# Kernel tuning notes

Measured on AMD Instinct MI355X. Metric: run time of the kernel, lower is better.

Reference implementation:

```python
import jax, jax.numpy as jnp
import numpy as np

HID = 768
NSPLITS = 12
HEAD_RATIO = 2
H = NSPLITS // HEAD_RATIO          # 6 attention heads
D = HID // NSPLITS                 # 64 head size
AH = H * D                         # 384 all_head_size
KS = 9                             # conv kernel size
PAD = (KS - 1) // 2
B, S = 4, 1024


def setup_inputs() -> dict:
    key = jax.random.key(0)
    ks = jax.random.split(key, 16)
    std = 0.02
    inp = {
        "Q": jax.random.normal(ks[0], (B, S, HID), jnp.float32),
        "K": jax.random.normal(ks[1], (B, S, HID), jnp.float32),
        "V": jax.random.normal(ks[2], (B, S, HID), jnp.float32),
        "td": jax.random.uniform(ks[3], (B, S), jnp.float32),
        "mask": jax.random.randint(ks[4], (B, S), 0, 2, jnp.int32),
        # projection weights, applied as x @ W (in, out)
        "Wq": jax.random.normal(ks[5], (HID, AH), jnp.float32) * std,
        "Wk": jax.random.normal(ks[6], (HID, AH), jnp.float32) * std,
        "Wv": jax.random.normal(ks[7], (HID, AH), jnp.float32) * std,
        # separable conv: depthwise (HID, KS), pointwise (AH, HID), bias (AH,)
        "dw_w": jax.random.normal(ks[8], (HID, KS), jnp.float32) * std,
        "pw_w": jax.random.normal(ks[9], (AH, HID), jnp.float32) * std,
        "sep_b": jnp.zeros((AH,), jnp.float32),
        # conv_kernel_layer Linear(AH -> H*KS)
        "ck_W": jax.random.normal(ks[10], (AH, H * KS), jnp.float32) * std,
        "ck_b": jnp.zeros((H * KS,), jnp.float32),
        # conv_out_layer Linear(HID -> AH)
        "co_W": jax.random.normal(ks[11], (HID, AH), jnp.float32) * std,
        "co_b": jnp.zeros((AH,), jnp.float32),
        # gammas init to zeros as in torch module
        "gammas": jnp.zeros((H, 1, 1), jnp.float32),
    }
    return inp


def dist_func(scores, td, am, gammas):
    # scores: [B,H,S,S]; am: [B,1,1,S] bool key mask; entirely non-differentiable.
    s = scores.shape[-1]
    dt = scores.dtype
    amf = am.astype(dt)
    p = jax.nn.softmax(jnp.where(am, scores, -1e8), axis=-1) * amf
    distcum = jnp.cumsum(p, axis=-1)
    disttotal = jnp.sum(p, axis=-1, keepdims=True)
    # |j - i| position distance
    pos = jnp.abs(jnp.arange(s)[None, :] - jnp.arange(s)[:, None]).astype(dt)
    dist_scores = jnp.sqrt(jnp.clip((disttotal - distcum) * pos[None, None], 0.0, None))
    gamma = -jax.nn.softplus(gammas)[None]  # (1,H,1,1)
    total_effect = jnp.clip(jnp.exp(dist_scores * gamma), 1e-5, 1e5)
    # time-distance effect on strictly-lower-triangular positions
    tdn = td / jnp.maximum(jnp.linalg.norm(td, axis=-1, keepdims=True), 1e-12)
    td_scores = jnp.broadcast_to(tdn[:, None, None, :], scores.shape)
    td_sm = jax.nn.softmax(jnp.where(am, td_scores, -1e4), axis=-1)
    lower = jnp.tril(jnp.ones((s, s), dt), -1)  # (triu == 0)
    return jax.lax.stop_gradient(total_effect - td_sm * lower[None, None])


def reference(Q, K, V, td, mask, Wq, Wk, Wv, dw_w, pw_w, sep_b, ck_W, ck_b, co_W, co_b, gammas):
    b, s, hid = Q.shape
    mq = Q @ Wq  # (B,S,AH)
    mk = K @ Wk
    mv = V @ Wv
    # SeparableConv1D over sequence dim of K
    x = jnp.transpose(K, (0, 2, 1))  # (B,HID,S)
    dw = jax.lax.conv_general_dilated(
        x, dw_w[:, None, :], window_strides=(1,), padding=[(PAD, PAD)],
        feature_group_count=hid, dimension_numbers=("NCH", "OIH", "NCH"))
    pw = jnp.einsum("bcs,oc->bos", dw, pw_w) + sep_b[None, :, None]
    mkc = jnp.transpose(pw, (0, 2, 1))  # (B,S,AH)

    q = mq.reshape(b, s, H, D).transpose(0, 2, 1, 3)
    k = mk.reshape(b, s, H, D).transpose(0, 2, 1, 3)
    v = mv.reshape(b, s, H, D).transpose(0, 2, 1, 3)

    # dynamic span convolution
    conv_attn = mkc * mq                                   # (B,S,AH)
    ck = (conv_attn @ ck_W + ck_b).reshape(b, s, H, KS)
    ck = jax.nn.softmax(ck, axis=-1)                       # per-position kernel
    co = V @ co_W + co_b                                   # (B,S,AH)
    co_pad = jnp.pad(co, ((0, 0), (PAD, PAD), (0, 0)))
    idx = jnp.arange(s)[:, None] + jnp.arange(KS)[None, :]  # (S,KS)
    unf = co_pad[:, idx, :].reshape(b, s, KS, H, D)         # sliding window gather
    conv_out = jnp.einsum("bskhd,bshk->bshd", unf, ck)      # (B,S,H,D)

    # attention with distance decay
    scores = jnp.einsum("bhid,bhjd->bhij", q, k) / np.float32(np.sqrt(D))
    am = (mask[:, None, None, :] != 0)  # (B,1,1,S) key mask
    total_effect = dist_func(scores, td, am, gammas)
    scores = jnp.where(am, scores * total_effect, -1e8)
    probs = jax.nn.softmax(scores, axis=-1)
    ctx = jnp.einsum("bhij,bhjd->bhid", probs, v).transpose(0, 2, 1, 3)  # (B,S,H,D)

    out = jnp.concatenate([ctx, conv_out], axis=2).reshape(b, s, HEAD_RATIO * AH)
    return out
```

## Files before the change

kernel.cpp:

```cpp
#include <hip/hip_runtime.h>
#include <hip/hip_bf16.h>

#define HIDC 768
#define Hh   6
#define Dd   64
#define AHc  384
#define KSc  9
#define PADc 4
#define Bb   4
#define Ss   1024
#define MRr  (Bb * Ss)

typedef __attribute__((ext_vector_type(8))) __bf16 bf16x8;
typedef __attribute__((ext_vector_type(4))) __bf16 bf16x4;
typedef __attribute__((ext_vector_type(4))) float  f32x4;

__device__ __forceinline__ void gl_lds16(const void* g, void* l) {
    __builtin_amdgcn_global_load_lds(
        (const __attribute__((address_space(1))) void*)g,
        (__attribute__((address_space(3))) void*)l, 16, 0, 0);
}

__device__ __forceinline__ void split8(const float* p, bf16x8& hi, bf16x8& lo) {
    float4 x0 = *(const float4*)p;
    float4 x1 = *(const float4*)(p + 4);
    float xs[8] = {x0.x, x0.y, x0.z, x0.w, x1.x, x1.y, x1.z, x1.w};
#pragma unroll
    for (int e = 0; e < 8; ++e) {
        __bf16 hv = (__bf16)xs[e];
        hi[e] = hv;
        lo[e] = (__bf16)(xs[e] - (float)hv);
    }
}

__device__ __forceinline__ void split8r(const float* xs, bf16x8& hi, bf16x8& lo) {
#pragma unroll
    for (int e = 0; e < 8; ++e) {
        __bf16 hv = (__bf16)xs[e];
        hi[e] = hv;
        lo[e] = (__bf16)(xs[e] - (float)hv);
    }
}

__device__ __forceinline__ bf16x8 cvt8(const float* p) {
    float4 x0 = *(const float4*)p;
    float4 x1 = *(const float4*)(p + 4);
    float xs[8] = {x0.x, x0.y, x0.z, x0.w, x1.x, x1.y, x1.z, x1.w};
    bf16x8 h;
#pragma unroll
    for (int e = 0; e < 8; ++e) h[e] = (__bf16)xs[e];
    return h;
}

__global__ __launch_bounds__(256) void k_pre(
        const float* __restrict__ Wq, const float* __restrict__ Wk,
        const float* __restrict__ Wv, const float* __restrict__ coW,
        const float* __restrict__ pww, const float* __restrict__ cob,
        const float* __restrict__ sepb, const float* __restrict__ td,
        const int* __restrict__ mask, const float* __restrict__ Kin,
        const float* __restrict__ dww, const float* __restrict__ Q,
        const float* __restrict__ V,
        __bf16* __restrict__ Whi, __bf16* __restrict__ Wlo,
        float* __restrict__ biasb, float* __restrict__ td_sm,
        __bf16* __restrict__ dwbf, __bf16* __restrict__ qbf,
        __bf16* __restrict__ vbf) {
    __shared__ float shmem[64 * 65];
    int bid = blockIdx.x;
    int tid = threadIdx.x;
    if (bid < 288) {
        int z = bid / 72, rem = bid % 72;
        int n0 = (rem % 6) * 64, k0 = (rem / 6) * 64;
        const float* src = (z == 0) ? Wq : (z == 1) ? Wk : (z == 2) ? Wv : coW;
        float (*tile)[65] = (float(*)[65])shmem;
        int r = tid >> 2, cq = tid & 3;
#pragma unroll
        for (int e = 0; e < 4; ++e) {
            float4 v = *(const float4*)&src[(size_t)(k0 + r) * AHc + n0 + cq * 16 + e * 4];
            tile[r][cq * 16 + e * 4 + 0] = v.x;
            tile[r][cq * 16 + e * 4 + 1] = v.y;
            tile[r][cq * 16 + e * 4 + 2] = v.z;
            tile[r][cq * 16 + e * 4 + 3] = v.w;
        }
        __syncthreads();
        float x[16];
#pragma unroll
        for (int e = 0; e < 16; ++e) x[e] = tile[cq * 16 + e][r];
        bf16x8 h0, l0, h1, l1;
        split8r(x, h0, l0);
        split8r(x + 8, h1, l1);
        size_t dst = ((size_t)(z * AHc + n0 + r)) * HIDC + k0 + cq * 16;
        *(bf16x8*)(Whi + dst)     = h0;
        *(bf16x8*)(Whi + dst + 8) = h1;
        *(bf16x8*)(Wlo + dst)     = l0;
        *(bf16x8*)(Wlo + dst + 8) = l1;
        return;
    }
    if (bid < 432) {
        int idx = (bid - 288) * 256 + tid;
        bf16x8 hi, lo;
        split8(pww + (size_t)idx * 8, hi, lo);
        size_t dst = (size_t)4 * AHc * HIDC + (size_t)idx * 8;
        *(bf16x8*)(Whi + dst) = hi;
        *(bf16x8*)(Wlo + dst) = lo;
        return;
    }
    if (bid < 440) {
        int idx = (bid - 432) * 256 + tid;
        if (idx < 5 * AHc) {
            int z = idx / AHc, n = idx % AHc;
            biasb[idx] = (z == 3) ? cob[n] : (z == 4) ? sepb[n] : 0.f;
        }
        return;
    }
    if (bid < 444) {
        int b = bid - 440;
        float* red = shmem;
        float* tv  = shmem + 256;
        float ls = 0.f;
        for (int j = tid; j < Ss; j += 256) {
            float v = td[b * Ss + j];
            tv[j] = v;
            ls += v * v;
        }
        red[tid] = ls; __syncthreads();
        for (int s = 128; s > 0; s >>= 1) { if (tid < s) red[tid] += red[tid + s]; __syncthreads(); }
        float norm = fmaxf(sqrtf(red[0]), 1e-12f);
        __syncthreads();
        float lm = -3e38f;
        for (int j = tid; j < Ss; j += 256) {
            float v = mask[b * Ss + j] ? tv[j] / norm : -1e4f;
            tv[j] = v;
            lm = fmaxf(lm, v);
        }
        red[tid] = lm; __syncthreads();
        for (int s = 128; s > 0; s >>= 1) { if (tid < s) red[tid] = fmaxf(red[tid], red[tid + s]); __syncthreads(); }
        float m = red[0]; __syncthreads();
        float lsum = 0.f;
        for (int j = tid; j < Ss; j += 256) {
            float e = expf(tv[j] - m);
            tv[j] = e;
            lsum += e;
        }
        red[tid] = lsum; __syncthreads();
        for (int s = 128; s > 0; s >>= 1) { if (tid < s) red[tid] += red[tid + s]; __syncthreads(); }
        float inv = 1.f / red[0];
        __syncthreads();
        for (int j = tid; j < Ss; j += 256)
            td_sm[b * Ss + j] = tv[j] * inv;
        return;
    }
    int db = bid - 444;
    if (db < 3072) {
        int idx = db * 256 + tid;
        int c4 = idx % (HIDC / 4);
        int s  = (idx / (HIDC / 4)) % Ss;
        int b  = idx / ((HIDC / 4) * Ss);
        int c  = c4 * 4;
        float wv[4][KSc];
#pragma unroll
        for (int j = 0; j < 4; ++j)
#pragma unroll
            for (int k = 0; k < KSc; ++k) wv[j][k] = dww[(c + j) * KSc + k];
        float4 acc = {0.f, 0.f, 0.f, 0.f};
#pragma unroll
        for (int k = 0; k < KSc; ++k) {
            int sp = s + k - PADc;
            if (sp >= 0 && sp < Ss) {
                float4 v = *(const float4*)&Kin[(size_t)(b * Ss + sp) * HIDC + c];
                acc.x += v.x * wv[0][k]; acc.y += v.y * wv[1][k];
                acc.z += v.z * wv[2][k]; acc.w += v.w * wv[3][k];
            }
        }
        bf16x4 o = {(__bf16)acc.x, (__bf16)acc.y, (__bf16)acc.z, (__bf16)acc.w};
        *(bf16x4*)(dwbf + (size_t)idx * 4) = o;
    } else {
        const int n8 = MRr * HIDC / 8;
        int idx = (db - 3072) * 256 + tid;
        if (idx < n8) {
            *(bf16x8*)(qbf + (size_t)idx * 8) = cvt8(Q + (size_t)idx * 8);
        } else {
            int i = idx - n8;
            *(bf16x8*)(vbf + (size_t)i * 8) = cvt8(V + (size_t)i * 8);
        }
    }
}

__global__ __launch_bounds__(256) void k_gemm5(
        const __bf16* __restrict__ qbf, const float* __restrict__ Kin,
        const __bf16* __restrict__ vbf, const __bf16* __restrict__ dwbf,
        const __bf16* __restrict__ Whi, const __bf16* __restrict__ Wlo,
        const float* __restrict__ biasb, float* __restrict__ Call,
        __bf16* __restrict__ kh, __bf16* __restrict__ kl,
        __bf16* __restrict__ qh, __bf16* __restrict__ vt) {
    __shared__ __attribute__((aligned(16))) __bf16 As [128 * 32];
    __shared__ __attribute__((aligned(16))) __bf16 BsH[128 * 32];
    __shared__ __attribute__((aligned(16))) __bf16 BsL[128 * 32];

    int wg = blockIdx.x + 3 * (blockIdx.y + 32 * blockIdx.z);
    int n2 = (wg & 7) * 60 + (wg >> 3);
    int bxx = n2 % 3, byy = (n2 / 3) % 32, z = n2 / 96;

    int m0 = byy * 128, n0 = bxx * 128;
    int tid = threadIdx.x;
    int wave = tid >> 6, lane = tid & 63, quad = lane >> 4, l15 = lane & 15;

    int lrow = lane >> 2;
    int lswz = 8 * ((lane & 3) ^ (lrow & 3));

    int brow = wave * 32 + lrow;
    const __bf16* BhG0 = Whi + ((size_t)(z * AHc + n0 + brow)) * HIDC + lswz;
    const __bf16* BhG1 = BhG0 + (size_t)16 * HIDC;
    const __bf16* BlG0 = Wlo + ((size_t)(z * AHc + n0 + brow)) * HIDC + lswz;
    const __bf16* BlG1 = BlG0 + (size_t)16 * HIDC;
    __bf16* BhL0 = BsH + (wave * 2 + 0) * 512;
    __bf16* BhL1 = BsH + (wave * 2 + 1) * 512;
    __bf16* BlL0 = BsL + (wave * 2 + 0) * 512;
    __bf16* BlL1 = BsL + (wave * 2 + 1) * 512;

    const __bf16* Abf = (z == 0) ? qbf : (z == 4) ? dwbf : vbf;
    const __bf16* AG0 = Abf + ((size_t)(m0 + wave * 32 + lrow)) * HIDC + lswz;
    const __bf16* AG1 = AG0 + (size_t)16 * HIDC;
    __bf16* AL0 = As + (wave * 2 + 0) * 512;
    __bf16* AL1 = As + (wave * 2 + 1) * 512;

    int sr = tid >> 1;
    int sk = (tid & 1) * 16;
    const float* Arow = Kin + (size_t)(m0 + sr) * HIDC + sk;
    int g0 = sk >> 3;
    int d0 = sr * 32 + ((g0       ^ (sr & 3)) * 8);
    int d1 = sr * 32 + (((g0 + 1) ^ (sr & 3)) * 8);

    int swz = (quad ^ (l15 & 3)) * 8;
    f32x4 acc[4][4] = {};

    for (int k0 = 0; k0 < HIDC; k0 += 32) {
        if (z == 1) {
            const float* ap = Arow + k0;
            *(bf16x8*)&As[d0] = cvt8(ap);
            *(bf16x8*)&As[d1] = cvt8(ap + 8);
        } else {
            gl_lds16(AG0 + k0, AL0);
            gl_lds16(AG1 + k0, AL1);
        }
        gl_lds16(BhG0 + k0, BhL0);
        gl_lds16(BhG1 + k0, BhL1);
        gl_lds16(BlG0 + k0, BlL0);
        gl_lds16(BlG1 + k0, BlL1);
        __syncthreads();

        int mrow = (wave >> 1) * 64 + l15;
        int nrow = (wave & 1) * 64 + l15;
        bf16x8 ah[4], bh[4], bl[4];
#pragma unroll
        for (int mt = 0; mt < 4; ++mt)
            ah[mt] = *(bf16x8*)&As[(mrow + mt * 16) * 32 + swz];
#pragma unroll
        for (int nt = 0; nt < 4; ++nt) {
            bh[nt] = *(bf16x8*)&BsH[(nrow + nt * 16) * 32 + swz];
            bl[nt] = *(bf16x8*)&BsL[(nrow + nt * 16) * 32 + swz];
        }
#pragma unroll
        for (int mt = 0; mt < 4; ++mt)
#pragma unroll
            for (int nt = 0; nt < 4; ++nt) {
                acc[mt][nt] = __builtin_amdgcn_mfma_f32_16x16x32_bf16(ah[mt], bh[nt], acc[mt][nt], 0, 0, 0);
                acc[mt][nt] = __builtin_amdgcn_mfma_f32_16x16x32_bf16(ah[mt], bl[nt], acc[mt][nt], 0, 0, 0);
            }
        __syncthreads();
    }

    if (z == 1) {
#pragma unroll
        for (int nt = 0; nt < 4; ++nt) {
            int n = n0 + (wave & 1) * 64 + nt * 16 + l15;
#pragma unroll
            for (int mt = 0; mt < 4; ++mt) {
#pragma unroll
                for (int r = 0; r < 4; ++r) {
                    int m = m0 + (wave >> 1) * 64 + mt * 16 + quad * 4 + r;
                    float v = acc[mt][nt][r];
                    __bf16 hv = (__bf16)v;
                    kh[(size_t)m * AHc + n] = hv;
                    kl[(size_t)m * AHc + n] = (__bf16)(v - (float)hv);
                }
            }
        }
    } else if (z == 2) {
        int b = m0 >> 10;
#pragma unroll
        for (int nt = 0; nt < 4; ++nt) {
            int n = (wave & 1) * 64 + nt * 16 + l15;
            int gn = n0 + n;
            int h = gn >> 6, d = gn & 63;
#pragma unroll
            for (int mt = 0; mt < 4; ++mt) {
                int m = m0 + (wave >> 1) * 64 + mt * 16 + quad * 4;
                int s = m & (Ss - 1);
                bf16x4 o = {(__bf16)acc[mt][nt][0], (__bf16)acc[mt][nt][1],
                            (__bf16)acc[mt][nt][2], (__bf16)acc[mt][nt][3]};
                *(bf16x4*)&vt[((size_t)((b * Hh + h) * Dd + d)) * Ss + s] = o;
            }
        }
    } else if (z == 0) {
#pragma unroll
        for (int nt = 0; nt < 4; ++nt) {
            int n = n0 + (wave & 1) * 64 + nt * 16 + l15;
#pragma unroll
            for (int mt = 0; mt < 4; ++mt) {
#pragma unroll
                for (int r = 0; r < 4; ++r) {
                    int m = m0 + (wave >> 1) * 64 + mt * 16 + quad * 4 + r;
                    float v = acc[mt][nt][r];
                    Call[(size_t)m * AHc + n] = v;
                    qh[(size_t)m * AHc + n] = (__bf16)v;
                }
            }
        }
    } else {
        float* Cz = Call + (size_t)z * MRr * AHc;
        const float* bz = biasb + z * AHc;
#pragma unroll
        for (int nt = 0; nt < 4; ++nt) {
            int n = n0 + (wave & 1) * 64 + nt * 16 + l15;
            float bias = bz[n];
#pragma unroll
            for (int mt = 0; mt < 4; ++mt) {
#pragma unroll
                for (int r = 0; r < 4; ++r) {
                    int m = m0 + (wave >> 1) * 64 + mt * 16 + quad * 4 + r;
                    Cz[(size_t)m * AHc + n] = acc[mt][nt][r] + bias;
                }
            }
        }
    }
}

__global__ __launch_bounds__(256) void k_ckconv(const float* __restrict__ mkc,
                                                const float* __restrict__ mq,
                                                const float* __restrict__ ckW,
                                                const float* __restrict__ ckb,
                                                const float* __restrict__ co,
                                                float* __restrict__ out) {
    int tid = threadIdx.x;
    int lr = tid >> 6, lane = tid & 63;
    int row = blockIdx.x * 4 + lr;
    __shared__ float ca[4][AHc];
    __shared__ float ckv[4][Hh * KSc];
    for (int o = lane; o < AHc; o += 64)
        ca[lr][o] = mkc[(size_t)row * AHc + o] * mq[(size_t)row * AHc + o];
    __syncthreads();
    if (lane < Hh * KSc) {
        float acc = ckb[lane];
        for (int o = 0; o < AHc; ++o)
            acc += ca[lr][o] * ckW[o * (Hh * KSc) + lane];
        ckv[lr][lane] = acc;
    }
    __syncthreads();
    if (lane < Hh) {
        float m = -3e38f;
#pragma unroll
        for (int k = 0; k < KSc; ++k) m = fmaxf(m, ckv[lr][lane * KSc + k]);
        float e[KSc];
        float s = 0.f;
#pragma unroll
        for (int k = 0; k < KSc; ++k) { e[k] = expf(ckv[lr][lane * KSc + k] - m); s += e[k]; }
        float inv = 1.f / s;
#pragma unroll
        for (int k = 0; k < KSc; ++k) ckv[lr][lane * KSc + k] = e[k] * inv;
    }
    __syncthreads();
#pragma unroll
    for (int e = 0; e < 2; ++e) {
        int it = e * 256 + tid;
        if (it >= 4 * (AHc / 4)) break;
        int r4i = it / (AHc / 4), dq = it % (AHc / 4);
        int h = dq >> 4, d4 = dq & 15;
        int row2 = blockIdx.x * 4 + r4i;
        int s = row2 & (Ss - 1), b = row2 >> 10;
        float4 acc = {0.f, 0.f, 0.f, 0.f};
#pragma unroll
        for (int k = 0; k < KSc; ++k) {
            int sp = s + k - PADc;
            if (sp >= 0 && sp < Ss) {
                float4 v = *(const float4*)&co[(size_t)(b * Ss + sp) * AHc + h * Dd + d4 * 4];
                float wv = ckv[r4i][h * KSc + k];
                acc.x += wv * v.x; acc.y += wv * v.y; acc.z += wv * v.z; acc.w += wv * v.w;
            }
        }
        *(float4*)&out[(size_t)row2 * (2 * AHc) + AHc + h * Dd + d4 * 4] = acc;
    }
}

__device__ __forceinline__ int scix(int m, int j) {
    return m * 1024 + (j ^ (((m ^ (j >> 6)) & 7) << 2));
}

__global__ __launch_bounds__(512, 4) void k_attn(const __bf16* __restrict__ qh,
                                              const __bf16* __restrict__ kh, const __bf16* __restrict__ kl,
                                              const __bf16* __restrict__ vt,
                                              const int* __restrict__ mask,
                                              const float* __restrict__ td_sm, const float* __restrict__ gammas,
                                              float* __restrict__ out) {
    __shared__ float sc[16 * 1024];
    int wg = blockIdx.x + 64 * blockIdx.y;
    int n  = (wg & 7) * 192 + (wg >> 3);
    int bx = n & 63, by = n >> 6;
    int i0 = bx * 16;
    int h = by % Hh, b = by / Hh;
    int tid = threadIdx.x;
    int w = tid >> 6, lane = tid & 63, quad = lane >> 4, l15 = lane & 15;
    int jw = w * 128;

    bf16x8 a_hi[2];
    {
        size_t qoff = (size_t)(b * Ss + i0 + l15) * AHc + h * Dd + quad * 8;
        a_hi[0] = *(const bf16x8*)(qh + qoff);
        a_hi[1] = *(const bf16x8*)(qh + qoff + 32);
    }
#pragma unroll 4
    for (int t = 0; t < 8; ++t) {
        int jt = jw + t * 16;
        size_t koff = (size_t)(b * Ss + jt + l15) * AHc + h * Dd + quad * 8;
        f32x4 acc = {0.f, 0.f, 0.f, 0.f};
#pragma unroll
        for (int kc = 0; kc < 2; ++kc) {
            bf16x8 khv = *(const bf16x8*)(kh + koff + kc * 32);
            bf16x8 klv = *(const bf16x8*)(kl + koff + kc * 32);
            acc = __builtin_amdgcn_mfma_f32_16x16x32_bf16(a_hi[kc], khv, acc, 0, 0, 0);
            acc = __builtin_amdgcn_mfma_f32_16x16x32_bf16(a_hi[kc], klv, acc, 0, 0, 0);
        }
#pragma unroll
        for (int r = 0; r < 4; ++r)
            sc[scix(quad * 4 + r, jt + l15)] = acc[r] * 0.125f;
    }
    __syncthreads();

    const int* mrow = mask + b * Ss;
    const float* tdrow = td_sm + b * Ss;
    float gamma = -log1pf(expf(gammas[h]));
    int jb = lane << 4;
    __attribute__((aligned(16))) int marr[16];
    {
        const int4* mp = (const int4*)(mrow + jb);
#pragma unroll
        for (int k = 0; k < 4; ++k) ((int4*)marr)[k] = mp[k];
    }
    __attribute__((aligned(16))) float tdv[16];
    {
        const float4* tp = (const float4*)(tdrow + jb);
#pragma unroll
        for (int k = 0; k < 4; ++k) ((float4*)tdv)[k] = tp[k];
    }

    {
        int mA = w * 2, mB = mA + 1;
        int iA = i0 + mA, iB = i0 + mB;
        __attribute__((aligned(16))) float sA[16], sB[16];
        float pA[16], pB[16];
#pragma unroll
        for (int g = 0; g < 4; ++g) {
            *(f32x4*)(sA + 4 * g) = *(const f32x4*)&sc[scix(mA, jb + 4 * g)];
            *(f32x4*)(sB + 4 * g) = *(const f32x4*)&sc[scix(mB, jb + 4 * g)];
        }
        float mxA = -1e30f, mxB = -1e30f;
#pragma unroll
        for (int jj = 0; jj < 16; ++jj) {
            mxA = fmaxf(mxA, marr[jj] ? sA[jj] : -1e30f);
            mxB = fmaxf(mxB, marr[jj] ? sB[jj] : -1e30f);
        }
#pragma unroll
        for (int d = 1; d < 64; d <<= 1) {
            mxA = fmaxf(mxA, __shfl_xor(mxA, d));
            mxB = fmaxf(mxB, __shfl_xor(mxB, d));
        }
#pragma unroll
        for (int jj = 0; jj < 16; ++jj) {
            pA[jj] = marr[jj] ? __expf(sA[jj] - mxA) : 0.f;
            pB[jj] = marr[jj] ? __expf(sB[jj] - mxB) : 0.f;
        }
#pragma unroll
        for (int jj = 1; jj < 16; ++jj) { pA[jj] += pA[jj - 1]; pB[jj] += pB[jj - 1]; }
        float tA = pA[15], tB = pB[15];
        float incA = tA, incB = tB;
#pragma unroll
        for (int dlt = 1; dlt < 64; dlt <<= 1) {
            float vA = __shfl_up(incA, dlt);
            float vB = __shfl_up(incB, dlt);
            if (lane >= dlt) { incA += vA; incB += vB; }
        }
        float offA = incA - tA, offB = incB - tB;
        float totA = __shfl(incA, 63), totB = __shfl(incB, 63);
        float invA = 1.f / fmaxf(totA, 1e-30f), invB = 1.f / fmaxf(totB, 1e-30f);
        float mx2A = -1e30f, mx2B = -1e30f;
#pragma unroll
        for (int jj = 0; jj < 16; ++jj) {
            int j = jb + jj;
            float cumA = pA[jj] + offA, cumB = pB[jj] + offB;
            float posA = fabsf((float)(j - iA));
            float posB = fabsf((float)(j - iB));
            float dsA = sqrtf(fmaxf((totA - cumA) * invA * posA, 0.f));
            float dsB = sqrtf(fmaxf((totB - cumB) * invB * posB, 0.f));
            float teA = fminf(fmaxf(__expf(dsA * gamma), 1e-5f), 1e5f);
            float teB = fminf(fmaxf(__expf(dsB * gamma), 1e-5f), 1e5f);
            float tdj = tdv[jj];
            float multA = teA - ((j < iA) ? tdj : 0.f);
            float multB = teB - ((j < iB) ? tdj : 0.f);
            float s2A = marr[jj] ? sA[jj] * multA : -1e8f;
            float s2B = marr[jj] ? sB[jj] * multB : -1e8f;
            sA[jj] = s2A; sB[jj] = s2B;
            mx2A = fmaxf(mx2A, s2A); mx2B = fmaxf(mx2B, s2B);
        }
#pragma unroll
        for (int d = 1; d < 64; d <<= 1) {
            mx2A = fmaxf(mx2A, __shfl_xor(mx2A, d));
            mx2B = fmaxf(mx2B, __shfl_xor(mx2B, d));
        }
        float smA = 0.f, smB = 0.f;
#pragma unroll
        for (int jj = 0; jj < 16; ++jj) {
            sA[jj] = __expf(sA[jj] - mx2A); smA += sA[jj];
            sB[jj] = __expf(sB[jj] - mx2B); smB += sB[jj];
        }
#pragma unroll
        for (int d = 1; d < 64; d <<= 1) {
            smA += __shfl_xor(smA, d);
            smB += __shfl_xor(smB, d);
        }
        float i2A = 1.f / smA, i2B = 1.f / smB;
#pragma unroll
        for (int jj = 0; jj < 16; ++jj) { sA[jj] *= i2A; sB[jj] *= i2B; }
#pragma unroll
        for (int g = 0; g < 4; ++g) {
            *(f32x4*)&sc[scix(mA, jb + 4 * g)] = *(const f32x4*)(sA + 4 * g);
            *(f32x4*)&sc[scix(mB, jb + 4 * g)] = *(const f32x4*)(sB + 4 * g);
        }
    }
    __syncthreads();

    f32x4 oacc[4] = {};
    const __bf16* vtb = vt + (size_t)(b * Hh + h) * Dd * Ss;
#pragma unroll
    for (int kc = 0; kc < 4; ++kc) {
        int j0 = jw + kc * 32 + quad * 8;
        __attribute__((aligned(16))) float x[8];
        *(f32x4*)x       = *(const f32x4*)&sc[scix(l15, j0)];
        *(f32x4*)(x + 4) = *(const f32x4*)&sc[scix(l15, j0 + 4)];
        bf16x8 p_hi, p_lo;
        split8r(x, p_hi, p_lo);
#pragma unroll
        for (int nt = 0; nt < 4; ++nt) {
            int d = nt * 16 + l15;
            bf16x8 vv = *(const bf16x8*)(vtb + (size_t)d * Ss + j0);
            oacc[nt] = __builtin_amdgcn_mfma_f32_16x16x32_bf16(p_hi, vv, oacc[nt], 0, 0, 0);
            oacc[nt] = __builtin_amdgcn_mfma_f32_16x16x32_bf16(p_lo, vv, oacc[nt], 0, 0, 0);
        }
    }
    __syncthreads();
#pragma unroll
    for (int nt = 0; nt < 4; ++nt)
#pragma unroll
        for (int r = 0; r < 4; ++r)
            sc[w * 1024 + (quad * 4 + r) * 64 + nt * 16 + l15] = oacc[nt][r];
    __syncthreads();
#pragma unroll
    for (int e = 0; e < 2; ++e) {
        int idx = e * 512 + tid;
        int m = idx >> 6, dd = idx & 63;
        float v = 0.f;
#pragma unroll
        for (int ww = 0; ww < 8; ++ww) v += sc[ww * 1024 + idx];
        out[(size_t)(b * Ss + i0 + m) * (2 * AHc) + h * Dd + dd] = v;
    }
}

extern "C" void kernel_launch(void* const* d_in, const int* in_sizes, int n_in,
                              void* d_out, int out_size, void* d_ws, size_t ws_size,
                              hipStream_t stream) {
    const float* Q    = (const float*)d_in[0];
    const float* Kin  = (const float*)d_in[1];
    const float* V    = (const float*)d_in[2];
    const float* td   = (const float*)d_in[3];
    const int*   mask = (const int*)d_in[4];
    const float* Wq   = (const float*)d_in[5];
    const float* Wk   = (const float*)d_in[6];
    const float* Wv   = (const float*)d_in[7];
    const float* dww  = (const float*)d_in[8];
    const float* pww  = (const float*)d_in[9];
    const float* sepb = (const float*)d_in[10];
    const float* ckW  = (const float*)d_in[11];
    const float* ckb  = (const float*)d_in[12];
    const float* coW  = (const float*)d_in[13];
    const float* cob  = (const float*)d_in[14];
    const float* gam  = (const float*)d_in[15];
    float* out = (float*)d_out;
    float* ws = (float*)d_ws;

    float* mq    = ws;
    float* mks   = mq    + (size_t)MRr * AHc;
    float* mvs   = mks   + (size_t)MRr * AHc;
    float* co    = mvs   + (size_t)MRr * AHc;
    float* mkc   = co    + (size_t)MRr * AHc;
    float* dwr   = mkc   + (size_t)MRr * AHc;
    float* tdsm  = dwr   + (size_t)MRr * HIDC;
    float* biasb = tdsm  + (size_t)Bb * Ss;

    __bf16* dwbf = (__bf16*)dwr;
    __bf16* qbf  = (__bf16*)(dwr + (size_t)MRr * HIDC / 2);
    __bf16* kh = (__bf16*)mks;
    __bf16* kl = kh + (size_t)MRr * AHc;
    __bf16* vt = (__bf16*)mvs;
    __bf16* qh = vt + (size_t)MRr * AHc;

    __bf16* Whi = (__bf16*)d_out;
    __bf16* Wlo = Whi + (size_t)5 * AHc * HIDC;
    __bf16* vbf = Wlo + (size_t)5 * AHc * HIDC;

    k_pre<<<6588, 256, 0, stream>>>(Wq, Wk, Wv, coW, pww, cob, sepb, td, mask,
                                    Kin, dww, Q, V, Whi, Wlo, biasb, tdsm,
                                    dwbf, qbf, vbf);

    dim3 gg(AHc / 128, MRr / 128, 5);
    k_gemm5<<<gg, 256, 0, stream>>>(qbf, Kin, vbf, dwbf, Whi, Wlo, biasb, mq, kh, kl, qh, vt);

    k_ckconv<<<MRr / 4, 256, 0, stream>>>(mkc, mq, ckW, ckb, co, out);

    dim3 ga(Ss / 16, Bb * Hh);
    k_attn<<<ga, 512, 0, stream>>>(qh, kh, kl, vt, mask, tdsm, gam, out);
}
```

Measured before the change: 272.6 us.

## Keep attention scores in registers and shrink LDS to small bounce buffers

The attention kernel now keeps the 16x1024 score tile in MFMA accumulator registers instead of a 64KB shared array. Softmax, cumulative-sum and distance-decay reductions are done with 16-lane shuffles plus small per-wave shared stats arrays and extra barriers. P is converted to the PV operand layout through a small swizzled per-wave bounce buffer, and the final cross-wave reduction is staged in two halves. The aim is to cut LDS footprint (raising occupancy) and LDS traffic, at the cost of more registers, more syncs and redundant per-element divides. The ck linear loop in the conv kernel is also unrolled.

```diff
diff --git a/kernel.cpp b/kernel.cpp
--- a/kernel.cpp
+++ b/kernel.cpp
@@ -351,8 +351,10 @@
     __syncthreads();
     if (lane < Hh * KSc) {
         float acc = ckb[lane];
+        const float* wp = ckW + lane;
+#pragma unroll 8
         for (int o = 0; o < AHc; ++o)
-            acc += ca[lr][o] * ckW[o * (Hh * KSc) + lane];
+            acc += ca[lr][o] * wp[o * (Hh * KSc)];
         ckv[lr][lane] = acc;
     }
     __syncthreads();
@@ -391,17 +393,14 @@
     }
 }
 
-__device__ __forceinline__ int scix(int m, int j) {
-    return m * 1024 + (j ^ (((m ^ (j >> 6)) & 7) << 2));
-}
-
 __global__ __launch_bounds__(512, 4) void k_attn(const __bf16* __restrict__ qh,
-                                              const __bf16* __restrict__ kh, const __bf16* __restrict__ kl,
-                                              const __bf16* __restrict__ vt,
-                                              const int* __restrict__ mask,
-                                              const float* __restrict__ td_sm, const float* __restrict__ gammas,
-                                              float* __restrict__ out) {
-    __shared__ float sc[16 * 1024];
+            const __bf16* __restrict__ kh, const __bf16* __restrict__ kl,
+            const __bf16* __restrict__ vt,
+            const int* __restrict__ mask,
+            const float* __restrict__ td_sm, const float* __restrict__ gammas,
+            float* __restrict__ out) {
+    __shared__ __attribute__((aligned(16))) float bounce[8][512];
+    __shared__ float statsM[128], statsS[128], stats2[128], statsZ[128];
     int wg = blockIdx.x + 64 * blockIdx.y;
     int n  = (wg & 7) * 192 + (wg >> 3);
     int bx = n & 63, by = n >> 6;
@@ -411,142 +410,202 @@
     int w = tid >> 6, lane = tid & 63, quad = lane >> 4, l15 = lane & 15;
     int jw = w * 128;
 
-    bf16x8 a_hi[2];
+    bf16x8 a_hi0, a_hi1;
     {
         size_t qoff = (size_t)(b * Ss + i0 + l15) * AHc + h * Dd + quad * 8;
-        a_hi[0] = *(const bf16x8*)(qh + qoff);
-        a_hi[1] = *(const bf16x8*)(qh + qoff + 32);
-    }
-#pragma unroll 4
+        a_hi0 = *(const bf16x8*)(qh + qoff);
+        a_hi1 = *(const bf16x8*)(qh + qoff + 32);
+    }
+    f32x4 sreg[8];
+#pragma unroll
     for (int t = 0; t < 8; ++t) {
-        int jt = jw + t * 16;
-        size_t koff = (size_t)(b * Ss + jt + l15) * AHc + h * Dd + quad * 8;
+        size_t koff = (size_t)(b * Ss + jw + t * 16 + l15) * AHc + h * Dd + quad * 8;
+        bf16x8 kh0 = *(const bf16x8*)(kh + koff);
+        bf16x8 kl0 = *(const bf16x8*)(kl + koff);
+        bf16x8 kh1 = *(const bf16x8*)(kh + koff + 32);
+        bf16x8 kl1 = *(const bf16x8*)(kl + koff + 32);
         f32x4 acc = {0.f, 0.f, 0.f, 0.f};
-#pragma unroll
-        for (int kc = 0; kc < 2; ++kc) {
-            bf16x8 khv = *(const bf16x8*)(kh + koff + kc * 32);
-            bf16x8 klv = *(const bf16x8*)(kl + koff + kc * 32);
-            acc = __builtin_amdgcn_mfma_f32_16x16x32_bf16(a_hi[kc], khv, acc, 0, 0, 0);
-            acc = __builtin_amdgcn_mfma_f32_16x16x32_bf16(a_hi[kc], klv, acc, 0, 0, 0);
-        }
+        acc = __builtin_amdgcn_mfma_f32_16x16x32_bf16(a_hi0, kh0, acc, 0, 0, 0);
+        acc = __builtin_amdgcn_mfma_f32_16x16x32_bf16(a_hi0, kl0, acc, 0, 0, 0);
+        acc = __builtin_amdgcn_mfma_f32_16x16x32_bf16(a_hi1, kh1, acc, 0, 0, 0);
+        acc = __builtin_amdgcn_mfma_f32_16x16x32_bf16(a_hi1, kl1, acc, 0, 0, 0);
+        sreg[t] = acc;
+    }
+
+    float gamma = -log1pf(expf(gammas[h]));
+    int mbits = 0;
+    float tdv[8];
+    {
+        const int* mp = mask + b * Ss + jw + l15;
+        const float* tp = td_sm + b * Ss + jw + l15;
+#pragma unroll
+        for (int t = 0; t < 8; ++t) {
+            mbits |= (mp[t * 16] != 0) << t;
+            tdv[t] = tp[t * 16];
+        }
+    }
+#pragma unroll
+    for (int t = 0; t < 8; ++t) {
+        bool bit = (mbits >> t) & 1;
 #pragma unroll
         for (int r = 0; r < 4; ++r)
-            sc[scix(quad * 4 + r, jt + l15)] = acc[r] * 0.125f;
-    }
-    __syncthreads();
-
-    const int* mrow = mask + b * Ss;
-    const float* tdrow = td_sm + b * Ss;
-    float gamma = -log1pf(expf(gammas[h]));
-    int jb = lane << 4;
-    __attribute__((aligned(16))) int marr[16];
+            sreg[t][r] = bit ? sreg[t][r] * 0.125f : -1e30f;
+    }
     {
-        const int4* mp = (const int4*)(mrow + jb);
-#pragma unroll
-        for (int k = 0; k < 4; ++k) ((int4*)marr)[k] = mp[k];
-    }
-    __attribute__((aligned(16))) float tdv[16];
+        float pm[4];
+#pragma unroll
+        for (int r = 0; r < 4; ++r) {
+            float m0 = sreg[0][r];
+#pragma unroll
+            for (int t = 1; t < 8; ++t) m0 = fmaxf(m0, sreg[t][r]);
+#pragma unroll
+            for (int d = 1; d < 16; d <<= 1) m0 = fmaxf(m0, __shfl_xor(m0, d));
+            pm[r] = m0;
+        }
+        if (l15 == 0) {
+#pragma unroll
+            for (int r = 0; r < 4; ++r) statsM[(quad * 4 + r) * 8 + w] = pm[r];
+        }
+    }
+    __syncthreads();
+    float gmx[4];
+#pragma unroll
+    for (int r = 0; r < 4; ++r) {
+        const float* sm = &statsM[(quad * 4 + r) * 8];
+        float m0 = sm[0];
+#pragma unroll
+        for (int w2 = 1; w2 < 8; ++w2) m0 = fmaxf(m0, sm[w2]);
+        gmx[r] = m0;
+    }
+    float p[8][4];
     {
-        const float4* tp = (const float4*)(tdrow + jb);
-#pragma unroll
-        for (int k = 0; k < 4; ++k) ((float4*)tdv)[k] = tp[k];
-    }
-
-    {
-        int mA = w * 2, mB = mA + 1;
-        int iA = i0 + mA, iB = i0 + mB;
-        __attribute__((aligned(16))) float sA[16], sB[16];
-        float pA[16], pB[16];
-#pragma unroll
-        for (int g = 0; g < 4; ++g) {
-            *(f32x4*)(sA + 4 * g) = *(const f32x4*)&sc[scix(mA, jb + 4 * g)];
-            *(f32x4*)(sB + 4 * g) = *(const f32x4*)&sc[scix(mB, jb + 4 * g)];
-        }
-        float mxA = -1e30f, mxB = -1e30f;
-#pragma unroll
-        for (int jj = 0; jj < 16; ++jj) {
-            mxA = fmaxf(mxA, marr[jj] ? sA[jj] : -1e30f);
-            mxB = fmaxf(mxB, marr[jj] ? sB[jj] : -1e30f);
-        }
-#pragma unroll
-        for (int d = 1; d < 64; d <<= 1) {
-            mxA = fmaxf(mxA, __shfl_xor(mxA, d));
-            mxB = fmaxf(mxB, __shfl_xor(mxB, d));
-        }
-#pragma unroll
-        for (int jj = 0; jj < 16; ++jj) {
-            pA[jj] = marr[jj] ? __expf(sA[jj] - mxA) : 0.f;
-            pB[jj] = marr[jj] ? __expf(sB[jj] - mxB) : 0.f;
-        }
-#pragma unroll
-        for (int jj = 1; jj < 16; ++jj) { pA[jj] += pA[jj - 1]; pB[jj] += pB[jj - 1]; }
-        float tA = pA[15], tB = pB[15];
-        float incA = tA, incB = tB;
-#pragma unroll
-        for (int dlt = 1; dlt < 64; dlt <<= 1) {
-            float vA = __shfl_up(incA, dlt);
-            float vB = __shfl_up(incB, dlt);
-            if (lane >= dlt) { incA += vA; incB += vB; }
-        }
-        float offA = incA - tA, offB = incB - tB;
-        float totA = __shfl(incA, 63), totB = __shfl(incB, 63);
-        float invA = 1.f / fmaxf(totA, 1e-30f), invB = 1.f / fmaxf(totB, 1e-30f);
-        float mx2A = -1e30f, mx2B = -1e30f;
-#pragma unroll
-        for (int jj = 0; jj < 16; ++jj) {
-            int j = jb + jj;
-            float cumA = pA[jj] + offA, cumB = pB[jj] + offB;
-            float posA = fabsf((float)(j - iA));
-            float posB = fabsf((float)(j - iB));
-            float dsA = sqrtf(fmaxf((totA - cumA) * invA * posA, 0.f));
-            float dsB = sqrtf(fmaxf((totB - cumB) * invB * posB, 0.f));
-            float teA = fminf(fmaxf(__expf(dsA * gamma), 1e-5f), 1e5f);
-            float teB = fminf(fmaxf(__expf(dsB * gamma), 1e-5f), 1e5f);
-            float tdj = tdv[jj];
-            float multA = teA - ((j < iA) ? tdj : 0.f);
-            float multB = teB - ((j < iB) ? tdj : 0.f);
-            float s2A = marr[jj] ? sA[jj] * multA : -1e8f;
-            float s2B = marr[jj] ? sB[jj] * multB : -1e8f;
-            sA[jj] = s2A; sB[jj] = s2B;
-            mx2A = fmaxf(mx2A, s2A); mx2B = fmaxf(mx2B, s2B);
-        }
-#pragma unroll
-        for (int d = 1; d < 64; d <<= 1) {
-            mx2A = fmaxf(mx2A, __shfl_xor(mx2A, d));
-            mx2B = fmaxf(mx2B, __shfl_xor(mx2B, d));
-        }
-        float smA = 0.f, smB = 0.f;
-#pragma unroll
-        for (int jj = 0; jj < 16; ++jj) {
-            sA[jj] = __expf(sA[jj] - mx2A); smA += sA[jj];
-            sB[jj] = __expf(sB[jj] - mx2B); smB += sB[jj];
-        }
-#pragma unroll
-        for (int d = 1; d < 64; d <<= 1) {
-            smA += __shfl_xor(smA, d);
-            smB += __shfl_xor(smB, d);
-        }
-        float i2A = 1.f / smA, i2B = 1.f / smB;
-#pragma unroll
-        for (int jj = 0; jj < 16; ++jj) { sA[jj] *= i2A; sB[jj] *= i2B; }
-#pragma unroll
-        for (int g = 0; g < 4; ++g) {
-            *(f32x4*)&sc[scix(mA, jb + 4 * g)] = *(const f32x4*)(sA + 4 * g);
-            *(f32x4*)&sc[scix(mB, jb + 4 * g)] = *(const f32x4*)(sB + 4 * g);
-        }
-    }
-    __syncthreads();
+        float wrow[4];
+#pragma unroll
+        for (int r = 0; r < 4; ++r) {
+            float run = 0.f;
+#pragma unroll
+            for (int t = 0; t < 8; ++t) {
+                float v = __expf(sreg[t][r] - gmx[r]);
+#pragma unroll
+                for (int d = 1; d < 16; d <<= 1) {
+                    float u = __shfl_up(v, d, 16);
+                    if (l15 >= d) v += u;
+                }
+                float ct = __shfl(v, 15, 16);
+                p[t][r] = v + run;
+                run += ct;
+            }
+            wrow[r] = run;
+        }
+        if (l15 == 0) {
+#pragma unroll
+            for (int r = 0; r < 4; ++r) statsS[(quad * 4 + r) * 8 + w] = wrow[r];
+        }
+    }
+    __syncthreads();
+    float woff[4], tot[4];
+#pragma unroll
+    for (int r = 0; r < 4; ++r) {
+        const float* ss = &statsS[(quad * 4 + r) * 8];
+        float o = 0.f, t_ = 0.f;
+#pragma unroll
+        for (int w2 = 0; w2 < 8; ++w2) {
+            float v = ss[w2];
+            if (w2 < w) o += v;
+            t_ += v;
+        }
+        woff[r] = o; tot[r] = t_;
+    }
+    float mx2[4] = {-1e30f, -1e30f, -1e30f, -1e30f};
+#pragma unroll
+    for (int t = 0; t < 8; ++t) {
+        int j = jw + t * 16 + l15;
+        int bit = (mbits >> t) & 1;
+#pragma unroll
+        for (int r = 0; r < 4; ++r) {
+            int i = i0 + quad * 4 + r;
+            float inv = 1.f / fmaxf(tot[r], 1e-30f);
+            float cum = p[t][r] + woff[r];
+            float pos = fabsf((float)(j - i));
+            float ds = sqrtf(fmaxf((tot[r] - cum) * inv * pos, 0.f));
+            float te = fminf(fmaxf(__expf(ds * gamma), 1e-5f), 1e5f);
+            float mult = te - ((j < i) ? tdv[t] : 0.f);
+            float s2 = bit ? sreg[t][r] * mult : -1e8f;
+            sreg[t][r] = s2;
+            mx2[r] = fmaxf(mx2[r], s2);
+        }
+    }
+#pragma unroll
+    for (int r = 0; r < 4; ++r) {
+#pragma unroll
+        for (int d = 1; d < 16; d <<= 1) mx2[r] = fmaxf(mx2[r], __shfl_xor(mx2[r], d));
+    }
+    if (l15 == 0) {
+#pragma unroll
+        for (int r = 0; r < 4; ++r) stats2[(quad * 4 + r) * 8 + w] = mx2[r];
+    }
+    __syncthreads();
+    float gm2[4];
+#pragma unroll
+    for (int r = 0; r < 4; ++r) {
+        const float* s2p = &stats2[(quad * 4 + r) * 8];
+        float m0 = s2p[0];
+#pragma unroll
+        for (int w2 = 1; w2 < 8; ++w2) m0 = fmaxf(m0, s2p[w2]);
+        gm2[r] = m0;
+    }
+    float smr[4] = {0.f, 0.f, 0.f, 0.f};
+#pragma unroll
+    for (int t = 0; t < 8; ++t)
+#pragma unroll
+        for (int r = 0; r < 4; ++r) {
+            float e = __expf(sreg[t][r] - gm2[r]);
+            sreg[t][r] = e;
+            smr[r] += e;
+        }
+#pragma unroll
+    for (int r = 0; r < 4; ++r) {
+#pragma unroll
+        for (int d = 1; d < 16; d <<= 1) smr[r] += __shfl_xor(smr[r], d);
+    }
+    if (l15 == 0) {
+#pragma unroll
+        for (int r = 0; r < 4; ++r) statsZ[(quad * 4 + r) * 8 + w] = smr[r];
+    }
+    __syncthreads();
+#pragma unroll
+    for (int r = 0; r < 4; ++r) {
+        const float* zp = &statsZ[(quad * 4 + r) * 8];
+        float z = 0.f;
+#pragma unroll
+        for (int w2 = 0; w2 < 8; ++w2) z += zp[w2];
+        float inv2 = 1.f / z;
+#pragma unroll
+        for (int t = 0; t < 8; ++t) sreg[t][r] *= inv2;
+    }
 
     f32x4 oacc[4] = {};
     const __bf16* vtb = vt + (size_t)(b * Hh + h) * Dd * Ss;
+    float* myb = &bounce[w][0];
 #pragma unroll
     for (int kc = 0; kc < 4; ++kc) {
-        int j0 = jw + kc * 32 + quad * 8;
+#pragma unroll
+        for (int half = 0; half < 2; ++half) {
+            int jl = half * 16 + l15;
+#pragma unroll
+            for (int r = 0; r < 4; ++r) {
+                int m = quad * 4 + r;
+                int gi = (jl >> 2) ^ (m & 7);
+                myb[m * 32 + gi * 4 + (jl & 3)] = sreg[kc * 2 + half][r];
+            }
+        }
+        __syncthreads();
         __attribute__((aligned(16))) float x[8];
-        *(f32x4*)x       = *(const f32x4*)&sc[scix(l15, j0)];
-        *(f32x4*)(x + 4) = *(const f32x4*)&sc[scix(l15, j0 + 4)];
+        *(f32x4*)x       = *(const f32x4*)&myb[l15 * 32 + (((quad * 2)     ^ (l15 & 7)) * 4)];
+        *(f32x4*)(x + 4) = *(const f32x4*)&myb[l15 * 32 + (((quad * 2 + 1) ^ (l15 & 7)) * 4)];
         bf16x8 p_hi, p_lo;
         split8r(x, p_hi, p_lo);
+        int j0 = jw + kc * 32 + quad * 8;
 #pragma unroll
         for (int nt = 0; nt < 4; ++nt) {
             int d = nt * 16 + l15;
@@ -554,21 +613,32 @@
             oacc[nt] = __builtin_amdgcn_mfma_f32_16x16x32_bf16(p_hi, vv, oacc[nt], 0, 0, 0);
             oacc[nt] = __builtin_amdgcn_mfma_f32_16x16x32_bf16(p_lo, vv, oacc[nt], 0, 0, 0);
         }
-    }
-    __syncthreads();
-#pragma unroll
-    for (int nt = 0; nt < 4; ++nt)
-#pragma unroll
-        for (int r = 0; r < 4; ++r)
-            sc[w * 1024 + (quad * 4 + r) * 64 + nt * 16 + l15] = oacc[nt][r];
+        __syncthreads();
+    }
+
+    float* seg = (float*)bounce;
+    if (w < 4) {
+#pragma unroll
+        for (int nt = 0; nt < 4; ++nt)
+#pragma unroll
+            for (int r = 0; r < 4; ++r)
+                seg[w * 1024 + (quad * 4 + r) * 64 + nt * 16 + l15] = oacc[nt][r];
+    }
+    __syncthreads();
+    if (w >= 4) {
+        int s4 = w - 4;
+#pragma unroll
+        for (int nt = 0; nt < 4; ++nt)
+#pragma unroll
+            for (int r = 0; r < 4; ++r)
+                seg[s4 * 1024 + (quad * 4 + r) * 64 + nt * 16 + l15] += oacc[nt][r];
+    }
     __syncthreads();
 #pragma unroll
     for (int e = 0; e < 2; ++e) {
         int idx = e * 512 + tid;
         int m = idx >> 6, dd = idx & 63;
-        float v = 0.f;
-#pragma unroll
-        for (int ww = 0; ww < 8; ++ww) v += sc[ww * 1024 + idx];
+        float v = seg[idx] + seg[1024 + idx] + seg[2048 + idx] + seg[3072 + idx];
         out[(size_t)(b * Ss + i0 + m) * (2 * AHc) + h * Dd + dd] = v;
     }
 }
```

Result: slower. 285.7 us (+4.8%).

## Merge dynamic-span conv into attention launch and pack key mask into bitmask

Applied to the files above, without the earlier changes.

The separate k_ckconv launch is removed. Its work now runs as extra blocks (blockIdx.y >= 24) of the attention kernel, with 8 rows per block and the shared score buffer reused for scratch. This saves a kernel launch and lets the conv blocks overlap with the attention blocks. In the attention path the 16-entry int mask array is packed into a bit mask, and masked scores are pre-set once, which cuts register use and per-element selects. The risk is that the conv blocks inherit the attention kernel's 512-thread shape and large LDS allocation, which could lower occupancy for that work.

```diff
diff --git a/kernel.cpp b/kernel.cpp
--- a/kernel.cpp
+++ b/kernel.cpp
@@ -335,79 +335,83 @@
     }
 }
 
-__global__ __launch_bounds__(256) void k_ckconv(const float* __restrict__ mkc,
-                                                const float* __restrict__ mq,
-                                                const float* __restrict__ ckW,
-                                                const float* __restrict__ ckb,
-                                                const float* __restrict__ co,
-                                                float* __restrict__ out) {
-    int tid = threadIdx.x;
-    int lr = tid >> 6, lane = tid & 63;
-    int row = blockIdx.x * 4 + lr;
-    __shared__ float ca[4][AHc];
-    __shared__ float ckv[4][Hh * KSc];
-    for (int o = lane; o < AHc; o += 64)
-        ca[lr][o] = mkc[(size_t)row * AHc + o] * mq[(size_t)row * AHc + o];
-    __syncthreads();
-    if (lane < Hh * KSc) {
-        float acc = ckb[lane];
-        for (int o = 0; o < AHc; ++o)
-            acc += ca[lr][o] * ckW[o * (Hh * KSc) + lane];
-        ckv[lr][lane] = acc;
-    }
-    __syncthreads();
-    if (lane < Hh) {
-        float m = -3e38f;
-#pragma unroll
-        for (int k = 0; k < KSc; ++k) m = fmaxf(m, ckv[lr][lane * KSc + k]);
-        float e[KSc];
-        float s = 0.f;
-#pragma unroll
-        for (int k = 0; k < KSc; ++k) { e[k] = expf(ckv[lr][lane * KSc + k] - m); s += e[k]; }
-        float inv = 1.f / s;
-#pragma unroll
-        for (int k = 0; k < KSc; ++k) ckv[lr][lane * KSc + k] = e[k] * inv;
-    }
-    __syncthreads();
-#pragma unroll
-    for (int e = 0; e < 2; ++e) {
-        int it = e * 256 + tid;
-        if (it >= 4 * (AHc / 4)) break;
-        int r4i = it / (AHc / 4), dq = it % (AHc / 4);
-        int h = dq >> 4, d4 = dq & 15;
-        int row2 = blockIdx.x * 4 + r4i;
-        int s = row2 & (Ss - 1), b = row2 >> 10;
-        float4 acc = {0.f, 0.f, 0.f, 0.f};
-#pragma unroll
-        for (int k = 0; k < KSc; ++k) {
-            int sp = s + k - PADc;
-            if (sp >= 0 && sp < Ss) {
-                float4 v = *(const float4*)&co[(size_t)(b * Ss + sp) * AHc + h * Dd + d4 * 4];
-                float wv = ckv[r4i][h * KSc + k];
-                acc.x += wv * v.x; acc.y += wv * v.y; acc.z += wv * v.z; acc.w += wv * v.w;
-            }
-        }
-        *(float4*)&out[(size_t)row2 * (2 * AHc) + AHc + h * Dd + d4 * 4] = acc;
-    }
-}
-
 __device__ __forceinline__ int scix(int m, int j) {
     return m * 1024 + (j ^ (((m ^ (j >> 6)) & 7) << 2));
 }
 
-__global__ __launch_bounds__(512, 4) void k_attn(const __bf16* __restrict__ qh,
-                                              const __bf16* __restrict__ kh, const __bf16* __restrict__ kl,
-                                              const __bf16* __restrict__ vt,
-                                              const int* __restrict__ mask,
-                                              const float* __restrict__ td_sm, const float* __restrict__ gammas,
-                                              float* __restrict__ out) {
+__global__ __attribute__((amdgpu_flat_work_group_size(512, 512), amdgpu_waves_per_eu(4, 4)))
+void k_attnck(const __bf16* __restrict__ qh,
+              const __bf16* __restrict__ kh, const __bf16* __restrict__ kl,
+              const __bf16* __restrict__ vt,
+              const int* __restrict__ mask,
+              const float* __restrict__ td_sm, const float* __restrict__ gammas,
+              const float* __restrict__ mkc, const float* __restrict__ mq,
+              const float* __restrict__ ckW, const float* __restrict__ ckb,
+              const float* __restrict__ co,
+              float* __restrict__ out) {
     __shared__ float sc[16 * 1024];
+    int tid = threadIdx.x;
+
+    if (blockIdx.y >= 24) {
+        int cb = blockIdx.x + 64 * (blockIdx.y - 24);
+        int lr = tid >> 6, lane = tid & 63;
+        int row = cb * 8 + lr;
+        float* ca  = sc;
+        float* ckv = sc + 8 * AHc;
+        for (int o = lane; o < AHc; o += 64)
+            ca[lr * AHc + o] = mkc[(size_t)row * AHc + o] * mq[(size_t)row * AHc + o];
+        __syncthreads();
+        if (lane < Hh * KSc) {
+            float acc = ckb[lane];
+            const float* wp = ckW + lane;
+#pragma unroll 8
+            for (int o = 0; o < AHc; ++o)
+                acc += ca[lr * AHc + o] * wp[o * (Hh * KSc)];
+            ckv[lr * (Hh * KSc) + lane] = acc;
+        }
+        __syncthreads();
+        if (lane < Hh) {
+            float m = -3e38f;
+#pragma unroll
+            for (int k = 0; k < KSc; ++k) m = fmaxf(m, ckv[lr * (Hh * KSc) + lane * KSc + k]);
+            float e[KSc];
+            float s = 0.f;
+#pragma unroll
+            for (int k = 0; k < KSc; ++k) { e[k] = expf(ckv[lr * (Hh * KSc) + lane * KSc + k] - m); s += e[k]; }
+            float inv = 1.f / s;
+#pragma unroll
+            for (int k = 0; k < KSc; ++k) ckv[lr * (Hh * KSc) + lane * KSc + k] = e[k] * inv;
+        }
+        __syncthreads();
+#pragma unroll
+        for (int e = 0; e < 2; ++e) {
+            int it = e * 512 + tid;
+            if (it < 8 * (AHc / 4)) {
+                int r8 = it / (AHc / 4), dq = it % (AHc / 4);
+                int h = dq >> 4, d4 = dq & 15;
+                int row2 = cb * 8 + r8;
+                int s = row2 & (Ss - 1), b = row2 >> 10;
+                float4 acc = {0.f, 0.f, 0.f, 0.f};
+#pragma unroll
+                for (int k = 0; k < KSc; ++k) {
+                    int sp = s + k - PADc;
+                    if (sp >= 0 && sp < Ss) {
+                        float4 v = *(const float4*)&co[(size_t)(b * Ss + sp) * AHc + h * Dd + d4 * 4];
+                        float wv = ckv[r8 * (Hh * KSc) + h * KSc + k];
+                        acc.x += wv * v.x; acc.y += wv * v.y; acc.z += wv * v.z; acc.w += wv * v.w;
+                    }
+                }
+                *(float4*)&out[(size_t)row2 * (2 * AHc) + AHc + h * Dd + d4 * 4] = acc;
+            }
+        }
+        return;
+    }
+
     int wg = blockIdx.x + 64 * blockIdx.y;
     int n  = (wg & 7) * 192 + (wg >> 3);
     int bx = n & 63, by = n >> 6;
     int i0 = bx * 16;
     int h = by % Hh, b = by / Hh;
-    int tid = threadIdx.x;
     int w = tid >> 6, lane = tid & 63, quad = lane >> 4, l15 = lane & 15;
     int jw = w * 128;
 
@@ -435,15 +439,20 @@
     }
     __syncthreads();
 
-    const int* mrow = mask + b * Ss;
     const float* tdrow = td_sm + b * Ss;
     float gamma = -log1pf(expf(gammas[h]));
     int jb = lane << 4;
-    __attribute__((aligned(16))) int marr[16];
+    int mbits = 0;
     {
-        const int4* mp = (const int4*)(mrow + jb);
-#pragma unroll
-        for (int k = 0; k < 4; ++k) ((int4*)marr)[k] = mp[k];
+        const int4* mp = (const int4*)(mask + b * Ss + jb);
+#pragma unroll
+        for (int k = 0; k < 4; ++k) {
+            int4 mv = mp[k];
+            mbits |= (mv.x != 0) << (4 * k + 0);
+            mbits |= (mv.y != 0) << (4 * k + 1);
+            mbits |= (mv.z != 0) << (4 * k + 2);
+            mbits |= (mv.w != 0) << (4 * k + 3);
+        }
     }
     __attribute__((aligned(16))) float tdv[16];
     {
@@ -462,11 +471,15 @@
             *(f32x4*)(sA + 4 * g) = *(const f32x4*)&sc[scix(mA, jb + 4 * g)];
             *(f32x4*)(sB + 4 * g) = *(const f32x4*)&sc[scix(mB, jb + 4 * g)];
         }
+#pragma unroll
+        for (int jj = 0; jj < 16; ++jj) {
+            if (!((mbits >> jj) & 1)) { sA[jj] = -1e30f; sB[jj] = -1e30f; }
+        }
         float mxA = -1e30f, mxB = -1e30f;
 #pragma unroll
         for (int jj = 0; jj < 16; ++jj) {
-            mxA = fmaxf(mxA, marr[jj] ? sA[jj] : -1e30f);
-            mxB = fmaxf(mxB, marr[jj] ? sB[jj] : -1e30f);
+            mxA = fmaxf(mxA, sA[jj]);
+            mxB = fmaxf(mxB, sB[jj]);
         }
 #pragma unroll
         for (int d = 1; d < 64; d <<= 1) {
@@ -475,8 +488,8 @@
         }
 #pragma unroll
         for (int jj = 0; jj < 16; ++jj) {
-            pA[jj] = marr[jj] ? __expf(sA[jj] - mxA) : 0.f;
-            pB[jj] = marr[jj] ? __expf(sB[jj] - mxB) : 0.f;
+            pA[jj] = __expf(sA[jj] - mxA);
+            pB[jj] = __expf(sB[jj] - mxB);
         }
 #pragma unroll
         for (int jj = 1; jj < 16; ++jj) { pA[jj] += pA[jj - 1]; pB[jj] += pB[jj - 1]; }
@@ -495,6 +508,7 @@
 #pragma unroll
         for (int jj = 0; jj < 16; ++jj) {
             int j = jb + jj;
+            int bit = (mbits >> jj) & 1;
             float cumA = pA[jj] + offA, cumB = pB[jj] + offB;
             float posA = fabsf((float)(j - iA));
             float posB = fabsf((float)(j - iB));
@@ -505,8 +519,8 @@
             float tdj = tdv[jj];
             float multA = teA - ((j < iA) ? tdj : 0.f);
             float multB = teB - ((j < iB) ? tdj : 0.f);
-            float s2A = marr[jj] ? sA[jj] * multA : -1e8f;
-            float s2B = marr[jj] ? sB[jj] * multB : -1e8f;
+            float s2A = bit ? sA[jj] * multA : -1e8f;
+            float s2B = bit ? sB[jj] * multB : -1e8f;
             sA[jj] = s2A; sB[jj] = s2B;
             mx2A = fmaxf(mx2A, s2A); mx2B = fmaxf(mx2B, s2B);
         }
@@ -622,8 +636,7 @@
     dim3 gg(AHc / 128, MRr / 128, 5);
     k_gemm5<<<gg, 256, 0, stream>>>(qbf, Kin, vbf, dwbf, Whi, Wlo, biasb, mq, kh, kl, qh, vt);
 
-    k_ckconv<<<MRr / 4, 256, 0, stream>>>(mkc, mq, ckW, ckb, co, out);
-
-    dim3 ga(Ss / 16, Bb * Hh);
-    k_attn<<<ga, 512, 0, stream>>>(qh, kh, kl, vt, mask, tdsm, gam, out);
-}
+    dim3 ga(64, 32);
+    k_attnck<<<ga, 512, 0, stream>>>(qh, kh, kl, vt, mask, tdsm, gam,
+                                     mkc, mq, ckW, ckb, co, out);
+}
```

Result: no change. 277.1 us (+1.6%).
